# Performance work log

Measured on AMD Instinct MI355X. Metric: run time of the kernel, lower is better.

The kernel has to match this reference:

```python
import jax, jax.numpy as jnp
import numpy as np
import math

N_HEADS = 16

def _layernorm(x, g, b):
    m = x.mean(-1, keepdims=True)
    v = ((x - m) ** 2).mean(-1, keepdims=True)
    return (x - m) * jax.lax.rsqrt(v + 1e-5) * g + b

def _project(x):
    # Poincare ball (c=1) projection: clip last-dim norm to 1 - eps
    max_norm = 1.0 - 1e-5
    n = jnp.linalg.norm(x, axis=-1, keepdims=True)
    return jnp.where(n > max_norm, x * (max_norm / jnp.maximum(n, 1e-12)), x)


def setup_inputs() -> dict:
    key = jax.random.key(0)
    ks = jax.random.split(key, 8)
    B, L, D = 2, 2048, 1024
    w = lambda k, s: jax.random.normal(k, s, jnp.float32) * 0.02
    return dict(
        x=jax.random.normal(ks[0], (B, L, D), jnp.float32),
        wq=w(ks[1], (D, D)), bq=jnp.zeros((D,), jnp.float32),
        wk=w(ks[2], (D, D)), bk=jnp.zeros((D,), jnp.float32),
        wv=w(ks[3], (D, D)), bv=jnp.zeros((D,), jnp.float32),
        wo=w(ks[4], (D, D)), bo=jnp.zeros((D,), jnp.float32),
        g1=jnp.ones((D,), jnp.float32), b1=jnp.zeros((D,), jnp.float32),
        g2=jnp.ones((D,), jnp.float32), b2=jnp.zeros((D,), jnp.float32),
        w1=w(ks[5], (4 * D, D)), bf1=jnp.zeros((4 * D,), jnp.float32),
        w2=w(ks[6], (D, 4 * D)), bf2=jnp.zeros((D,), jnp.float32),
    )


def reference(x, wq, bq, wk, bk, wv, bv, wo, bo, g1, b1, g2, b2, w1, bf1, w2, bf2):
    B, L, D = x.shape
    H = N_HEADS
    hd = D // H
    temp = math.sqrt(hd)

    xn = _layernorm(x, g1, b1)

    def heads(w, b):
        y = xn @ w.T + b                       # [B, L, D]
        return y.reshape(B, L, H, hd).transpose(0, 2, 1, 3)  # [B, H, L, hd]

    q = _project(heads(wq, bq))
    k = _project(heads(wk, bk))
    v = heads(wv, bv)

    # -||q - k||^2 / temp, via ||q||^2 + ||k||^2 - 2 q.k (same math as the
    # explicit broadcast-diff in the torch code, expressed as a GEMM)
    q2 = (q ** 2).sum(-1)[..., :, None]        # [B, H, L, 1]
    k2 = (k ** 2).sum(-1)[..., None, :]        # [B, H, 1, L]
    qk = jnp.einsum('bhld,bhmd->bhlm', q, k)   # [B, H, L, L]
    scores = -(q2 + k2 - 2.0 * qk) / temp
    attn = jax.nn.softmax(scores, axis=-1)     # dropout = identity (eval mode)

    out = jnp.einsum('bhlm,bhmd->bhld', attn, v)
    out = out.transpose(0, 2, 1, 3).reshape(B, L, D) @ wo.T + bo

    x = _project(x + out)
    xn2 = _layernorm(x, g2, b2)
    h = jax.nn.gelu(xn2 @ w1.T + bf1, approximate=False)  # torch nn.GELU = erf
    x = _project(x + (h @ w2.T + bf2))
    return x
```

## Files before the change

### kernel.cpp

```cpp
#include <hip/hip_runtime.h>
#include <math.h>

#define SEQ_L 2048
#define DM    1024
#define NH    16
#define HD    64
#define BL    4096
#define DFF   4096
#define QKV_S 3072

typedef __attribute__((ext_vector_type(8))) short short8;
typedef __attribute__((ext_vector_type(4))) short s16x4;
typedef __attribute__((ext_vector_type(4))) float f32x4;

__device__ __forceinline__ short f2bf(float x) {
    unsigned u = __float_as_uint(x);
    u += 0x7fff + ((u >> 16) & 1);
    return (short)(u >> 16);
}
__device__ __forceinline__ float bf2f(short s) {
    return __uint_as_float(((unsigned)(unsigned short)s) << 16);
}

__device__ __forceinline__ float gelu_fast(float x) {
    const float xa = fabsf(x);
    const float z = xa * 0.70710678118654752440f;
    const float t = __builtin_amdgcn_rcpf(fmaf(0.3275911f, z, 1.f));
    float P = fmaf(t, 1.061405429f, -1.453152027f);
    P = fmaf(t, P, 1.421413741f);
    P = fmaf(t, P, -0.284496736f);
    P = fmaf(t, P, 0.254829592f);
    P *= t;
    const float e = __expf(-z * z);
    const float erfp = fmaf(-P, e, 1.f);
    return 0.5f * fmaf(xa, erfp, x);
}

__device__ __forceinline__ float block_sum(float v, float* red, int tid) {
#pragma unroll
    for (int m = 32; m; m >>= 1) v += __shfl_xor(v, m);
    if ((tid & 63) == 0) red[tid >> 6] = v;
    __syncthreads();
    v = red[0] + red[1] + red[2] + red[3];
    __syncthreads();
    return v;
}

__global__ __launch_bounds__(256) void cvt6_kernel(
    const float* __restrict__ wq, const float* __restrict__ wk,
    const float* __restrict__ wv, const float* __restrict__ wo,
    const float* __restrict__ w1, const float* __restrict__ w2,
    short* __restrict__ dst) {
    const size_t i = (size_t)blockIdx.x * 256 + threadIdx.x;
    const float* src;
    size_t off;
    if (i < 1048576) {
        const int seg = (int)(i >> 18);
        off = i & 262143;
        src = seg == 0 ? wq : seg == 1 ? wk : seg == 2 ? wv : wo;
    } else if (i < 2097152) { src = w1; off = i - 1048576; }
    else                    { src = w2; off = i - 2097152; }
    const float4 v = ((const float4*)src)[off];
    const s16x4 o = {f2bf(v.x), f2bf(v.y), f2bf(v.z), f2bf(v.w)};
    ((s16x4*)dst)[i] = o;
}

__global__ __launch_bounds__(256) void ln_bf16_kernel(const float* __restrict__ x,
                                                      const float* __restrict__ g,
                                                      const float* __restrict__ b,
                                                      short* __restrict__ out) {
    const int row = blockIdx.x;
    const int tid = threadIdx.x;
    __shared__ float red[4];
    const float4 xv = *(const float4*)(x + (size_t)row * DM + tid * 4);
    float s = xv.x + xv.y + xv.z + xv.w;
    s = block_sum(s, red, tid);
    const float mean = s * (1.f / (float)DM);
    float dx0 = xv.x - mean, dx1 = xv.y - mean, dx2 = xv.z - mean, dx3 = xv.w - mean;
    float ss = dx0 * dx0 + dx1 * dx1 + dx2 * dx2 + dx3 * dx3;
    ss = block_sum(ss, red, tid);
    const float rs = 1.f / sqrtf(ss * (1.f / (float)DM) + 1e-5f);
    const float4 gv = *(const float4*)(g + tid * 4);
    const float4 bv = *(const float4*)(b + tid * 4);
    const s16x4 ob = {f2bf(dx0 * rs * gv.x + bv.x), f2bf(dx1 * rs * gv.y + bv.y),
                      f2bf(dx2 * rs * gv.z + bv.z), f2bf(dx3 * rs * gv.w + bv.w)};
    *(s16x4*)(out + (size_t)row * DM + tid * 4) = ob;
}

__global__ __launch_bounds__(256) void resproj3_kernel(const float* __restrict__ a,
                                                       const float* __restrict__ c0,
                                                       const float* __restrict__ c1,
                                                       float* __restrict__ out) {
    const int row = blockIdx.x;
    const int tid = threadIdx.x;
    __shared__ float red[4];
    const float4 av = *(const float4*)(a + (size_t)row * DM + tid * 4);
    const float4 c0v = *(const float4*)(c0 + (size_t)row * DM + tid * 4);
    const float4 c1v = *(const float4*)(c1 + (size_t)row * DM + tid * 4);
    float4 sv;
    sv.x = av.x + c0v.x + c1v.x;
    sv.y = av.y + c0v.y + c1v.y;
    sv.z = av.z + c0v.z + c1v.z;
    sv.w = av.w + c0v.w + c1v.w;
    float ss = sv.x * sv.x + sv.y * sv.y + sv.z * sv.z + sv.w * sv.w;
    ss = block_sum(ss, red, tid);
    const float n = sqrtf(ss);
    const float mx = 1.f - 1e-5f;
    const float scale = (n > mx) ? (mx / fmaxf(n, 1e-12f)) : 1.f;
    sv.x *= scale; sv.y *= scale; sv.z *= scale; sv.w *= scale;
    *(float4*)(out + (size_t)row * DM + tid * 4) = sv;
}

__global__ __launch_bounds__(256) void qk_prep(const short* __restrict__ qkvB,
                                               short* __restrict__ Qb,
                                               short* __restrict__ Kb,
                                               float* __restrict__ k2) {
    const int tid = threadIdx.x, lane = tid & 63;
    const int vec = blockIdx.x * 4 + (tid >> 6);
    const int row = vec >> 4, h = vec & 15;
    const int b = row >> 11, l = row & 2047;
    const size_t dstv = ((size_t)(b * NH + h) * SEQ_L + l) * HD + lane;
    const float mx = 1.f - 1e-5f;
    {
        const float v = bf2f(qkvB[(size_t)row * QKV_S + h * HD + lane]);
        float s = v * v;
#pragma unroll
        for (int m = 32; m; m >>= 1) s += __shfl_xor(s, m);
        const float n = sqrtf(s);
        const float sc = (n > mx) ? (mx / fmaxf(n, 1e-12f)) : 1.f;
        Qb[dstv] = f2bf(v * sc);
    }
    {
        const float v = bf2f(qkvB[(size_t)row * QKV_S + DM + h * HD + lane]);
        float s = v * v;
#pragma unroll
        for (int m = 32; m; m >>= 1) s += __shfl_xor(s, m);
        const float n = sqrtf(s);
        const float sc = (n > mx) ? (mx / fmaxf(n, 1e-12f)) : 1.f;
        Kb[dstv] = f2bf(v * sc);
        if (lane == 0) k2[(size_t)(b * NH + h) * SEQ_L + l] = s * sc * sc * 0.125f;
    }
}

__global__ __launch_bounds__(256) void v_prep(const short* __restrict__ qkvB,
                                              short* __restrict__ Vtb) {
    const int blk = blockIdx.x;
    const int bh = blk >> 5, kt = blk & 31;
    const int b = bh >> 4, h = bh & 15;
    __shared__ short T[64 * 72];
    const int tid = threadIdx.x;
    {
        const int key = tid >> 2, ch = (tid & 3) * 16;
        const size_t src = ((size_t)b * SEQ_L + kt * 64 + key) * QKV_S + 2 * DM + h * HD + ch;
        *(short8*)&T[key * 72 + ch]     = *(const short8*)(qkvB + src);
        *(short8*)&T[key * 72 + ch + 8] = *(const short8*)(qkvB + src + 8);
    }
    __syncthreads();
    const int hd = tid >> 2, kc = (tid & 3) * 16;
    short8 o0, o1;
#pragma unroll
    for (int j = 0; j < 8; ++j) {
        o0[j] = T[(kc + j) * 72 + hd];
        o1[j] = T[(kc + 8 + j) * 72 + hd];
    }
    short* dst = Vtb + ((size_t)bh * HD + hd) * SEQ_L + kt * 64 + kc;
    *(short8*)dst = o0;
    *(short8*)(dst + 8) = o1;
}

template <int BM, int ACT, int OUTBF, int FUSED>
__global__ __launch_bounds__(256) void gemm_mfma(
    const short* __restrict__ A, const short* __restrict__ Bw,
    const float* __restrict__ bb0, const float* __restrict__ bb1,
    const float* __restrict__ bb2, void* __restrict__ Cout,
    void* __restrict__ Cout1, int M, int N, int K, int Kst) {
    constexpr int RT = BM / 32;
    constexpr bool VEPI = (OUTBF != 0);
    constexpr int RPW = BM / 2;
    constexpr int SMEM_STAGE = (BM * 32 + 128 * 32) * 2;
    constexpr int SMEM_EPI = 4 * RPW * 72 * 2;
    constexpr int SMEM_BYTES = VEPI ? (SMEM_EPI > SMEM_STAGE ? SMEM_EPI : SMEM_STAGE)
                                    : SMEM_STAGE;
    __shared__ __align__(16) char raw[SMEM_BYTES];
    short* As = (short*)raw;
    short* Bs = As + BM * 32;
    const int tid = threadIdx.x;
    const int wv = tid >> 6, lane = tid & 63;

    const int lid = blockIdx.x + gridDim.x * blockIdx.y;
    const int xcd = lid & 7, seq = lid >> 3;
    const int NX = gridDim.x;
    const int mg = gridDim.y >> 3;
    const int m0 = (xcd * mg + seq / NX) * BM;
    const int n0 = (seq % NX) * 128;

    const int zz = blockIdx.z;
    const int koff = zz * K;
    const int wr = (wv & 1) * (BM / 2);
    const int wc = (wv >> 1) * 64;

    const int arow = wv * (BM / 4) + (lane >> 2);
    const int brow = wv * 32 + (lane >> 2);
    const short* Ag = A + (size_t)(m0 + arow) * Kst + koff + (lane & 3) * 8;
    const short* Bg = Bw + (size_t)(n0 + brow) * Kst + koff + (lane & 3) * 8;
    short* AsW = As + (wv * (BM / 4)) * 32 + lane * 8;
    short* AsW2 = AsW + 16 * 32;
    short* BsW = Bs + (wv * 32) * 32 + lane * 8;
    short* BsW2 = BsW + 16 * 32;

    const f32x4 z4 = {0.f, 0.f, 0.f, 0.f};
    f32x4 acc[RT][4];
#pragma unroll
    for (int r = 0; r < RT; ++r)
#pragma unroll
        for (int c = 0; c < 4; ++c) acc[r][c] = z4;

    const int lrow = lane & 15, kq = (lane >> 4) * 8;

    short8 ra0, ra1, rb0, rb1;
    ra0 = *(const short8*)(Ag);
    if constexpr (BM == 128) ra1 = *(const short8*)(Ag + (size_t)16 * Kst);
    rb0 = *(const short8*)(Bg);
    rb1 = *(const short8*)(Bg + (size_t)16 * Kst);

    for (int kt = 0; kt < K; kt += 32) {
        __syncthreads();
        *(short8*)AsW = ra0;
        if constexpr (BM == 128) *(short8*)AsW2 = ra1;
        *(short8*)BsW = rb0;
        *(short8*)BsW2 = rb1;
        short8 na0, na1, nb0, nb1;
        if (kt + 32 < K) {
            na0 = *(const short8*)(Ag + kt + 32);
            if constexpr (BM == 128) na1 = *(const short8*)(Ag + (size_t)16 * Kst + kt + 32);
            nb0 = *(const short8*)(Bg + kt + 32);
            nb1 = *(const short8*)(Bg + (size_t)16 * Kst + kt + 32);
        }
        __syncthreads();
        short8 af[RT], bf[4];
#pragma unroll
        for (int r = 0; r < RT; ++r)
            af[r] = *(const short8*)&As[(wr + r * 16 + lrow) * 32 + kq];
#pragma unroll
        for (int c = 0; c < 4; ++c)
            bf[c] = *(const short8*)&Bs[(wc + c * 16 + lrow) * 32 + kq];
#pragma unroll
        for (int r = 0; r < RT; ++r)
#pragma unroll
            for (int c = 0; c < 4; ++c)
                acc[r][c] = __builtin_amdgcn_mfma_f32_16x16x32_bf16(af[r], bf[c], acc[r][c], 0, 0, 0);
        ra0 = na0; ra1 = na1; rb0 = nb0; rb1 = nb1;
    }

    const int col = lane & 15, rb = (lane >> 4) * 4;
    if constexpr (VEPI) {
        __syncthreads();
        short* Ot = (short*)raw + wv * (RPW * 72);
#pragma unroll
        for (int c = 0; c < 4; ++c) {
            const int gn = n0 + wc + c * 16 + col;
            float bias;
            if constexpr (FUSED) {
                const int seg = gn >> 10;
                bias = (seg == 0 ? bb0 : seg == 1 ? bb1 : bb2)[gn & 1023];
            } else {
                bias = bb0[gn];
            }
#pragma unroll
            for (int r = 0; r < RT; ++r)
#pragma unroll
                for (int i = 0; i < 4; ++i) {
                    float v = acc[r][c][i] + bias;
                    if constexpr (ACT) v = gelu_fast(v);
                    Ot[(r * 16 + rb + i) * 72 + c * 16 + col] = f2bf(v);
                }
        }
        if constexpr (BM == 128) {
            const int orow = lane >> 3, oc = (lane & 7) * 8;
#pragma unroll
            for (int it = 0; it < 8; ++it) {
                const short8 vv = *(const short8*)&Ot[(it * 8 + orow) * 72 + oc];
                *(short8*)((short*)Cout + (size_t)(m0 + wr + it * 8 + orow) * N + n0 + wc + oc) = vv;
            }
        } else {
            const int erow = lane >> 1, ec = (lane & 1) * 32;
            const short8 r0 = *(const short8*)&Ot[erow * 72 + ec + 0];
            const short8 r1 = *(const short8*)&Ot[erow * 72 + ec + 8];
            const short8 r2 = *(const short8*)&Ot[erow * 72 + ec + 16];
            const short8 r3 = *(const short8*)&Ot[erow * 72 + ec + 24];
            short* dst = (short*)Cout + (size_t)(m0 + wr + erow) * N + n0 + wc + ec;
            *(short8*)(dst + 0)  = r0;
            *(short8*)(dst + 8)  = r1;
            *(short8*)(dst + 16) = r2;
            *(short8*)(dst + 24) = r3;
        }
    } else {
        float* outp = (float*)(zz ? Cout1 : Cout);
#pragma unroll
        for (int c = 0; c < 4; ++c) {
            const int gn = n0 + wc + c * 16 + col;
            float bias;
            if constexpr (FUSED) {
                const int seg = gn >> 10;
                bias = (seg == 0 ? bb0 : seg == 1 ? bb1 : bb2)[gn & 1023];
            } else {
                bias = bb0[gn];
            }
            if (zz) bias = 0.f;
#pragma unroll
            for (int r = 0; r < RT; ++r) {
                const int gm = m0 + wr + r * 16 + rb;
#pragma unroll
                for (int i = 0; i < 4; ++i) {
                    float v = acc[r][c][i] + bias;
                    if constexpr (ACT) v = gelu_fast(v);
                    outp[(size_t)(gm + i) * N + gn] = v;
                }
            }
        }
    }
}

__global__ __launch_bounds__(256) void attn_mfma2(const short* __restrict__ Qb,
                                                  const short* __restrict__ Kb,
                                                  const short* __restrict__ Vtb,
                                                  const float* __restrict__ k2v,
                                                  short* __restrict__ aO) {
    const int qt = blockIdx.x, h = blockIdx.y, b = blockIdx.z;
    const int tid = threadIdx.x, wv = tid >> 6, lane = tid & 63;
    const int bh = b * NH + h;
    __shared__ __align__(16) short smem[2 * 64 * 72];
    short* Ks = smem;
    short* Vt = smem + 64 * 72;
    const int lrow = lane & 15, q8 = (lane >> 4) * 8, q4 = (lane >> 4) * 4;

    const short* Qh = Qb + (size_t)bh * SEQ_L * HD;
    const short* Kh = Kb + (size_t)bh * SEQ_L * HD;
    const short* Vh = Vtb + (size_t)bh * HD * SEQ_L;
    const float* k2p = k2v + (size_t)bh * SEQ_L;

    short8 qf[2][2];
#pragma unroll
    for (int nt = 0; nt < 2; ++nt)
#pragma unroll
        for (int kc = 0; kc < 2; ++kc)
            qf[nt][kc] = *(const short8*)(Qh +
                (size_t)(qt * 128 + wv * 32 + nt * 16 + lrow) * HD + kc * 32 + q8);

    const f32x4 z4 = {0.f, 0.f, 0.f, 0.f};
    f32x4 o[4][2];
#pragma unroll
    for (int ht = 0; ht < 4; ++ht)
#pragma unroll
        for (int nt = 0; nt < 2; ++nt) o[ht][nt] = z4;
    float lsum[2] = {0.f, 0.f};

    const int srow = tid >> 2, sch = (tid & 3) * 16;

    for (int kt = 0; kt < SEQ_L / 64; ++kt) {
        const int k0 = kt * 64;
        __syncthreads();
        {
            const short* g = Kh + (size_t)(k0 + srow) * HD + sch;
            *(short8*)&Ks[srow * 72 + sch]     = *(const short8*)g;
            *(short8*)&Ks[srow * 72 + sch + 8] = *(const short8*)(g + 8);
            const short* gv = Vh + (size_t)srow * SEQ_L + k0 + sch;
            *(short8*)&Vt[srow * 72 + sch]     = *(const short8*)gv;
            *(short8*)&Vt[srow * 72 + sch + 8] = *(const short8*)(gv + 8);
        }
        __syncthreads();

        short8 p8[2][2];
#pragma unroll
        for (int mt = 0; mt < 4; ++mt) {
            const short8 kf0 = *(const short8*)&Ks[(mt * 16 + lrow) * 72 + q8];
            const short8 kf1 = *(const short8*)&Ks[(mt * 16 + lrow) * 72 + 32 + q8];
            const float4 kk = *(const float4*)(k2p + k0 + mt * 16 + q4);
            const int c = mt >> 1, hi = (mt & 1) * 4;
#pragma unroll
            for (int nt = 0; nt < 2; ++nt) {
                f32x4 s = z4;
                s = __builtin_amdgcn_mfma_f32_16x16x32_bf16(kf0, qf[nt][0], s, 0, 0, 0);
                s = __builtin_amdgcn_mfma_f32_16x16x32_bf16(kf1, qf[nt][1], s, 0, 0, 0);
#pragma unroll
                for (int i = 0; i < 4; ++i) {
                    const float kki = (i == 0) ? kk.x : (i == 1) ? kk.y : (i == 2) ? kk.z : kk.w;
                    const float p = __expf(fmaf(s[i], 0.25f, -kki));
                    lsum[nt] += p;
                    p8[nt][c][hi + i] = f2bf(p);
                }
            }
        }
#pragma unroll
        for (int ht = 0; ht < 4; ++ht) {
#pragma unroll
            for (int c = 0; c < 2; ++c) {
                const s16x4 va = *(const s16x4*)&Vt[(ht * 16 + lrow) * 72 + c * 32 + q4];
                const s16x4 vb = *(const s16x4*)&Vt[(ht * 16 + lrow) * 72 + c * 32 + 16 + q4];
                const short8 v8 = {va[0], va[1], va[2], va[3], vb[0], vb[1], vb[2], vb[3]};
#pragma unroll
                for (int nt = 0; nt < 2; ++nt)
                    o[ht][nt] = __builtin_amdgcn_mfma_f32_16x16x32_bf16(v8, p8[nt][c], o[ht][nt], 0, 0, 0);
            }
        }
    }

#pragma unroll
    for (int nt = 0; nt < 2; ++nt) {
        lsum[nt] += __shfl_xor(lsum[nt], 16);
        lsum[nt] += __shfl_xor(lsum[nt], 32);
    }
    const float inv0 = 1.f / lsum[0], inv1 = 1.f / lsum[1];

    __syncthreads();
    short* Ot = smem + wv * (32 * 72);
#pragma unroll
    for (int ht = 0; ht < 4; ++ht)
#pragma unroll
        for (int nt = 0; nt < 2; ++nt) {
            const float iv = nt ? inv1 : inv0;
            const s16x4 ov = {f2bf(o[ht][nt][0] * iv), f2bf(o[ht][nt][1] * iv),
                              f2bf(o[ht][nt][2] * iv), f2bf(o[ht][nt][3] * iv)};
            *(s16x4*)&Ot[(nt * 16 + lrow) * 72 + ht * 16 + q4] = ov;
        }
    const int erow = lane >> 1, ec = (lane & 1) * 32;
    const short8 r0 = *(const short8*)&Ot[erow * 72 + ec + 0];
    const short8 r1 = *(const short8*)&Ot[erow * 72 + ec + 8];
    const short8 r2 = *(const short8*)&Ot[erow * 72 + ec + 16];
    const short8 r3 = *(const short8*)&Ot[erow * 72 + ec + 24];
    short* dst = aO + ((size_t)b * SEQ_L + qt * 128 + wv * 32 + erow) * DM + h * HD + ec;
    *(short8*)(dst + 0)  = r0;
    *(short8*)(dst + 8)  = r1;
    *(short8*)(dst + 16) = r2;
    *(short8*)(dst + 24) = r3;
}

extern "C" void kernel_launch(void* const* d_in, const int* in_sizes, int n_in,
                              void* d_out, int out_size, void* d_ws, size_t ws_size,
                              hipStream_t stream) {
    const float* x   = (const float*)d_in[0];
    const float* wq  = (const float*)d_in[1];
    const float* bq  = (const float*)d_in[2];
    const float* wk  = (const float*)d_in[3];
    const float* bk  = (const float*)d_in[4];
    const float* wv  = (const float*)d_in[5];
    const float* bv  = (const float*)d_in[6];
    const float* wo  = (const float*)d_in[7];
    const float* bo  = (const float*)d_in[8];
    const float* g1  = (const float*)d_in[9];
    const float* b1  = (const float*)d_in[10];
    const float* g2  = (const float*)d_in[11];
    const float* b2  = (const float*)d_in[12];
    const float* w1  = (const float*)d_in[13];
    const float* bf1 = (const float*)d_in[14];
    const float* w2  = (const float*)d_in[15];
    const float* bf2 = (const float*)d_in[16];
    float* out = (float*)d_out;

    char* base = (char*)d_ws;
    short* wbf  = (short*)base;
    short* qkvB = (short*)(base + (24u << 20));
    short* xnb  = (short*)(base + (48u << 20));
    short* Qb   = xnb;
    short* Kb   = (short*)(base + (56u << 20));
    short* Vtb  = (short*)(base + (64u << 20));
    float* k2   = (float*)(base + (72u << 20));
    short* aO   = (short*)(base + (72u << 20) + (256u << 10));
    float* Pa   = (float*)(base + (24u << 20));
    float* Pb   = (float*)(base + (41u << 20));
    short* xn2b = Vtb;
    short* hbuf = qkvB;
    float* Ya   = (float*)base;
    float* Yb   = (float*)(base + (58u << 20));

    cvt6_kernel<<<12288, 256, 0, stream>>>(wq, wk, wv, wo, w1, w2, wbf);
    ln_bf16_kernel<<<BL, 256, 0, stream>>>(x, g1, b1, xnb);
    gemm_mfma<64, 0, 1, 1><<<dim3(24, 64), 256, 0, stream>>>(
        xnb, wbf, bq, bk, bv, qkvB, nullptr, BL, QKV_S, DM, DM);
    qk_prep<<<16384, 256, 0, stream>>>(qkvB, Qb, Kb, k2);
    v_prep<<<1024, 256, 0, stream>>>(qkvB, Vtb);
    attn_mfma2<<<dim3(16, 16, 2), 256, 0, stream>>>(Qb, Kb, Vtb, k2, aO);
    gemm_mfma<64, 0, 0, 0><<<dim3(8, 64, 2), 256, 0, stream>>>(
        aO, wbf + 3145728, bo, bo, bo, Pa, Pb, BL, DM, DM / 2, DM);
    resproj3_kernel<<<BL, 256, 0, stream>>>(x, Pa, Pb, out);
    ln_bf16_kernel<<<BL, 256, 0, stream>>>(out, g2, b2, xn2b);
    gemm_mfma<64, 1, 1, 0><<<dim3(32, 64), 256, 0, stream>>>(
        xn2b, wbf + 4194304, bf1, bf1, bf1, hbuf, nullptr, BL, DFF, DM, DM);
    gemm_mfma<64, 0, 0, 0><<<dim3(8, 64, 2), 256, 0, stream>>>(
        hbuf, wbf + 8388608, bf2, bf2, bf2, Ya, Yb, BL, DM, DFF / 2, DFF);
    resproj3_kernel<<<BL, 256, 0, stream>>>(out, Ya, Yb, out);
}
```

Before: 429.0 us.

## Use 128-row tiles for QKV and FFN1 GEMMs with chunked bf16 epilogue

Switches the QKV projection and FFN-up GEMMs from 64-row to 128-row tiles, halving the grid and increasing per-block reuse of B tiles. The bf16 epilogue is restructured to stage output through LDS in 32-row chunks, keeping the shared-memory footprint fixed, and bias loads are hoisted out of the row loop. An SWZ template flag disables the XCD block-swizzle for these launches and keeps it for the split-K fp32 GEMMs. Bigger tiles raise register pressure and reduce block count, which may lower occupancy.

```diff
diff --git a/kernel.cpp b/kernel.cpp
--- a/kernel.cpp
+++ b/kernel.cpp
@@ -168,7 +168,7 @@
     *(short8*)(dst + 8) = o1;
 }
 
-template <int BM, int ACT, int OUTBF, int FUSED>
+template <int BM, int ACT, int OUTBF, int FUSED, int SWZ>
 __global__ __launch_bounds__(256) void gemm_mfma(
     const short* __restrict__ A, const short* __restrict__ Bw,
     const float* __restrict__ bb0, const float* __restrict__ bb1,
@@ -176,9 +176,8 @@
     void* __restrict__ Cout1, int M, int N, int K, int Kst) {
     constexpr int RT = BM / 32;
     constexpr bool VEPI = (OUTBF != 0);
-    constexpr int RPW = BM / 2;
     constexpr int SMEM_STAGE = (BM * 32 + 128 * 32) * 2;
-    constexpr int SMEM_EPI = 4 * RPW * 72 * 2;
+    constexpr int SMEM_EPI = 4 * 32 * 72 * 2;
     constexpr int SMEM_BYTES = VEPI ? (SMEM_EPI > SMEM_STAGE ? SMEM_EPI : SMEM_STAGE)
                                     : SMEM_STAGE;
     __shared__ __align__(16) char raw[SMEM_BYTES];
@@ -187,12 +186,18 @@
     const int tid = threadIdx.x;
     const int wv = tid >> 6, lane = tid & 63;
 
-    const int lid = blockIdx.x + gridDim.x * blockIdx.y;
-    const int xcd = lid & 7, seq = lid >> 3;
-    const int NX = gridDim.x;
-    const int mg = gridDim.y >> 3;
-    const int m0 = (xcd * mg + seq / NX) * BM;
-    const int n0 = (seq % NX) * 128;
+    int m0, n0;
+    if constexpr (SWZ) {
+        const int lid = blockIdx.x + gridDim.x * blockIdx.y;
+        const int xcd = lid & 7, seq = lid >> 3;
+        const int NX = gridDim.x;
+        const int mg = gridDim.y >> 3;
+        m0 = (xcd * mg + seq / NX) * BM;
+        n0 = (seq % NX) * 128;
+    } else {
+        m0 = blockIdx.y * BM;
+        n0 = blockIdx.x * 128;
+    }
 
     const int zz = blockIdx.z;
     const int koff = zz * K;
@@ -255,40 +260,38 @@
     const int col = lane & 15, rb = (lane >> 4) * 4;
     if constexpr (VEPI) {
         __syncthreads();
-        short* Ot = (short*)raw + wv * (RPW * 72);
+        short* Ot = (short*)raw + wv * (32 * 72);
+        float bias[4];
 #pragma unroll
         for (int c = 0; c < 4; ++c) {
             const int gn = n0 + wc + c * 16 + col;
-            float bias;
             if constexpr (FUSED) {
                 const int seg = gn >> 10;
-                bias = (seg == 0 ? bb0 : seg == 1 ? bb1 : bb2)[gn & 1023];
+                bias[c] = (seg == 0 ? bb0 : seg == 1 ? bb1 : bb2)[gn & 1023];
             } else {
-                bias = bb0[gn];
-            }
-#pragma unroll
-            for (int r = 0; r < RT; ++r)
-#pragma unroll
-                for (int i = 0; i < 4; ++i) {
-                    float v = acc[r][c][i] + bias;
-                    if constexpr (ACT) v = gelu_fast(v);
-                    Ot[(r * 16 + rb + i) * 72 + c * 16 + col] = f2bf(v);
-                }
-        }
-        if constexpr (BM == 128) {
-            const int orow = lane >> 3, oc = (lane & 7) * 8;
-#pragma unroll
-            for (int it = 0; it < 8; ++it) {
-                const short8 vv = *(const short8*)&Ot[(it * 8 + orow) * 72 + oc];
-                *(short8*)((short*)Cout + (size_t)(m0 + wr + it * 8 + orow) * N + n0 + wc + oc) = vv;
-            }
-        } else {
-            const int erow = lane >> 1, ec = (lane & 1) * 32;
+                bias[c] = bb0[gn];
+            }
+        }
+        const int erow = lane >> 1, ec = (lane & 1) * 32;
+#pragma unroll
+        for (int p = 0; p < RT / 2; ++p) {
+#pragma unroll
+            for (int rr = 0; rr < 2; ++rr) {
+                const int r = p * 2 + rr;
+#pragma unroll
+                for (int c = 0; c < 4; ++c)
+#pragma unroll
+                    for (int i = 0; i < 4; ++i) {
+                        float v = acc[r][c][i] + bias[c];
+                        if constexpr (ACT) v = gelu_fast(v);
+                        Ot[(rr * 16 + rb + i) * 72 + c * 16 + col] = f2bf(v);
+                    }
+            }
             const short8 r0 = *(const short8*)&Ot[erow * 72 + ec + 0];
             const short8 r1 = *(const short8*)&Ot[erow * 72 + ec + 8];
             const short8 r2 = *(const short8*)&Ot[erow * 72 + ec + 16];
             const short8 r3 = *(const short8*)&Ot[erow * 72 + ec + 24];
-            short* dst = (short*)Cout + (size_t)(m0 + wr + erow) * N + n0 + wc + ec;
+            short* dst = (short*)Cout + (size_t)(m0 + wr + p * 32 + erow) * N + n0 + wc + ec;
             *(short8*)(dst + 0)  = r0;
             *(short8*)(dst + 8)  = r1;
             *(short8*)(dst + 16) = r2;
@@ -475,18 +478,18 @@
 
     cvt6_kernel<<<12288, 256, 0, stream>>>(wq, wk, wv, wo, w1, w2, wbf);
     ln_bf16_kernel<<<BL, 256, 0, stream>>>(x, g1, b1, xnb);
-    gemm_mfma<64, 0, 1, 1><<<dim3(24, 64), 256, 0, stream>>>(
+    gemm_mfma<128, 0, 1, 1, 0><<<dim3(24, 32), 256, 0, stream>>>(
         xnb, wbf, bq, bk, bv, qkvB, nullptr, BL, QKV_S, DM, DM);
     qk_prep<<<16384, 256, 0, stream>>>(qkvB, Qb, Kb, k2);
     v_prep<<<1024, 256, 0, stream>>>(qkvB, Vtb);
     attn_mfma2<<<dim3(16, 16, 2), 256, 0, stream>>>(Qb, Kb, Vtb, k2, aO);
-    gemm_mfma<64, 0, 0, 0><<<dim3(8, 64, 2), 256, 0, stream>>>(
+    gemm_mfma<64, 0, 0, 0, 1><<<dim3(8, 64, 2), 256, 0, stream>>>(
         aO, wbf + 3145728, bo, bo, bo, Pa, Pb, BL, DM, DM / 2, DM);
     resproj3_kernel<<<BL, 256, 0, stream>>>(x, Pa, Pb, out);
     ln_bf16_kernel<<<BL, 256, 0, stream>>>(out, g2, b2, xn2b);
-    gemm_mfma<64, 1, 1, 0><<<dim3(32, 64), 256, 0, stream>>>(
+    gemm_mfma<128, 1, 1, 0, 0><<<dim3(32, 32), 256, 0, stream>>>(
         xn2b, wbf + 4194304, bf1, bf1, bf1, hbuf, nullptr, BL, DFF, DM, DM);
-    gemm_mfma<64, 0, 0, 0><<<dim3(8, 64, 2), 256, 0, stream>>>(
+    gemm_mfma<64, 0, 0, 0, 1><<<dim3(8, 64, 2), 256, 0, stream>>>(
         hbuf, wbf + 8388608, bf2, bf2, bf2, Ya, Yb, BL, DM, DFF / 2, DFF);
     resproj3_kernel<<<BL, 256, 0, stream>>>(out, Ya, Yb, out);
 }
```

Result: faster. 418.3 us (-2.5%).
